# Optimization experiments

Hardware: AMD Instinct MI355X
Metric: run time of the kernel (lower is better)

The kernel has to match this reference:

```python
import jax, jax.numpy as jnp
import numpy as np

# Config constants (match init_kwargs)
D_MODEL = 1024
N_EXPERTS = 8
EXPERT_SCALE = 2          # experts per base group -> n_base_groups = 4
N_FEAT = 16
BANK_DIM = 32
RAW_FEAT = N_FEAT * BANK_DIM   # 512
PROJ_DIM = 256
R_HIDDEN = 256
E_HIDDEN = 256
TOP_K = 2
TEMP = 1.0
LN_EPS = 1e-5


def _layernorm(x, g, b):
    mu = jnp.mean(x, axis=-1, keepdims=True)
    var = jnp.mean((x - mu) ** 2, axis=-1, keepdims=True)
    return (x - mu) * jax.lax.rsqrt(var + LN_EPS) * g + b


def _softmax_top_k(logits, k):
    # keep top-k logits, mask rest to -inf, softmax
    topv = jax.lax.top_k(logits, k)[0]
    thresh = topv[..., -1:]
    masked = jnp.where(logits >= thresh, logits, -jnp.inf)
    return jax.nn.softmax(masked, axis=-1)


def setup_inputs() -> dict:
    key = jax.random.key(0)
    ks = jax.random.split(key, 24)
    B, S = 4, 2048
    s = 0.02
    inp = {
        "hidden": jax.random.normal(ks[0], (B, S, D_MODEL), jnp.float32),
        "feat": jax.random.normal(ks[1], (B, S, N_FEAT), jnp.float32),
        "feat_bank": jax.random.normal(ks[2], (B, S, N_FEAT, BANK_DIM), jnp.float32),
        "item_seq_len": jax.random.randint(ks[3], (B,), 1, S + 1, jnp.int64),
        # pre-LN
        "ln_g": jnp.ones((D_MODEL,), jnp.float32),
        "ln_b": jnp.zeros((D_MODEL,), jnp.float32),
        # router feature projector (2 layers: Linear -> GELU -> Linear)
        "fp_w1": jax.random.normal(ks[4], (RAW_FEAT, PROJ_DIM), jnp.float32) * s,
        "fp_b1": jnp.zeros((PROJ_DIM,), jnp.float32),
        "fp_w2": jax.random.normal(ks[5], (PROJ_DIM, PROJ_DIM), jnp.float32) * s,
        "fp_b2": jnp.zeros((PROJ_DIM,), jnp.float32),
        # learned router MLP: d_in = d_model + proj_dim
        "r_w1": jax.random.normal(ks[6], (D_MODEL + PROJ_DIM, R_HIDDEN), jnp.float32) * s,
        "r_b1": jnp.zeros((R_HIDDEN,), jnp.float32),
        "r_w2": jax.random.normal(ks[7], (R_HIDDEN, N_EXPERTS), jnp.float32) * s,
        "r_b2": jnp.zeros((N_EXPERTS,), jnp.float32),
        # rule router (linear on raw stage features)
        "rr_w": jax.random.normal(ks[8], (N_FEAT, N_EXPERTS), jnp.float32) * s,
        "rr_b": jnp.zeros((N_EXPERTS,), jnp.float32),
        # per-expert FFN
        "e_w1": jax.random.normal(ks[9], (N_EXPERTS, D_MODEL, E_HIDDEN), jnp.float32) * s,
        "e_b1": jnp.zeros((N_EXPERTS, E_HIDDEN), jnp.float32),
        "e_w2": jax.random.normal(ks[10], (N_EXPERTS, E_HIDDEN, D_MODEL), jnp.float32) * s,
        "e_b2": jnp.zeros((N_EXPERTS, D_MODEL), jnp.float32),
        "alpha": jnp.ones((), jnp.float32),
    }
    return inp


def reference(hidden, feat, feat_bank, item_seq_len, ln_g, ln_b,
              fp_w1, fp_b1, fp_w2, fp_b2,
              r_w1, r_b1, r_w2, r_b2,
              rr_w, rr_b,
              e_w1, e_b1, e_w2, e_b2, alpha):
    B, S, D = hidden.shape
    h_norm = _layernorm(hidden, ln_g, ln_b)  # [B,S,D]

    # router feature path: flatten bank, 2-layer GELU projector
    bank_flat = feat_bank.reshape(B, S, RAW_FEAT)
    proj = jnp.dot(jax.nn.gelu(jnp.dot(bank_flat, fp_w1) + fp_b1), fp_w2) + fp_b2  # [B,S,P]

    # token-mode router input: concat hidden + projected features
    router_input = jnp.concatenate([h_norm, proj], axis=-1)
    rule_logits = jnp.dot(feat, rr_w) + rr_b  # rule router on raw stage features

    raw_logits = jnp.dot(jax.nn.gelu(jnp.dot(router_input, r_w1) + r_b1), r_w2) + r_b2
    scaled_logits = raw_logits / max(TEMP, 1e-6)
    gate_weights = _softmax_top_k(scaled_logits, TOP_K)           # [B,S,E]
    rule_target_logits = rule_logits / max(TEMP, 1e-6)

    # expert group: per-expert 2-layer GELU FFN on h_norm
    h1 = jax.nn.gelu(jnp.einsum('bsd,edh->bseh', h_norm, e_w1) + e_b1)
    expert_out = jnp.einsum('bseh,ehd->bsed', h1, e_w2) + e_b2    # [B,S,E,D]

    stage_out = jnp.einsum('bse,bsed->bsd', gate_weights, expert_out)
    next_hidden = hidden + alpha * stage_out

    # _aggregate_group_weights: expert_group_idx = arange(E)//EXPERT_SCALE is
    # contiguous, so gather+sum per group == reshape+sum over the scale axis
    n_groups = N_EXPERTS // EXPERT_SCALE
    group_weights = gate_weights.reshape(B, S, n_groups, EXPERT_SCALE).sum(-1)

    return (next_hidden, stage_out, gate_weights, scaled_logits, group_weights, rule_target_logits)
```

## Files before the change

### kernel.cpp

```cpp
#include <hip/hip_runtime.h>
#include <stdint.h>


typedef unsigned short u16;
using bf16x8 = __attribute__((ext_vector_type(8))) short;
using f32x4  = __attribute__((ext_vector_type(4))) float;

#define WS_HHI 0u
#define WS_HLO 16777216u
#define WS_PB2 33554432u
#define WS_W1T 67108864u
#define WS_IDX 71303168u
#define IX_SELE   0u
#define IX_SELG   65536u
#define IX_ROW    131072u
#define IX_TOKR   196608u
#define IX_GROW   262144u
#define IX_CNT    327680u
#define IX_CBASE  335872u
#define IX_TILEE  344064u
#define IX_TILES  344704u
#define IX_TILEC  345344u
#define IX_META   345984u

__device__ __forceinline__ float gelu_tanh(float x) {
  float x3 = x * x * x;
  float t = tanhf(0.7978845608028654f * (x + 0.044715f * x3));
  return 0.5f * x * (1.0f + t);
}
__device__ __forceinline__ u16 f2bf(float f) {
  uint32_t u = __float_as_uint(f);
  u = u + 0x7fffu + ((u >> 16) & 1u);
  return (u16)(u >> 16);
}
__device__ __forceinline__ float b2f(u16 h) {
  return __uint_as_float(((uint32_t)h) << 16);
}
__device__ __forceinline__ void gll16(const void* g, void* l) {
  __builtin_amdgcn_global_load_lds(
      (const __attribute__((address_space(1))) void*)g,
      (__attribute__((address_space(3))) void*)l, 16, 0, 0);
}

__global__ __launch_bounds__(256) void split_bank_kernel(const float* __restrict__ x,
    u16* __restrict__ hi, u16* __restrict__ lo) {
  int i4 = blockIdx.x * 256 + threadIdx.x;
  float4 v = ((const float4*)x)[i4];
  ushort4 h, l;
  h.x = f2bf(v.x); l.x = f2bf(v.x - b2f(h.x));
  h.y = f2bf(v.y); l.y = f2bf(v.y - b2f(h.y));
  h.z = f2bf(v.z); l.z = f2bf(v.z - b2f(h.z));
  h.w = f2bf(v.w); l.w = f2bf(v.w - b2f(h.w));
  ((ushort4*)hi)[i4] = h;
  ((ushort4*)lo)[i4] = l;
}

__global__ __launch_bounds__(256) void tsplit_kernel(const float* __restrict__ in,
    int inR, int inC, u16* __restrict__ outHi, u16* __restrict__ outLo,
    int outLD, int outColOff) {
  __shared__ u16 hs[64][65];
  __shared__ u16 ls[64][65];
  int tid = threadIdx.x;
  int c0 = blockIdx.x * 64, r0 = blockIdx.y * 64;
  const float* inp = in + (size_t)blockIdx.z * inR * inC;
  int rl = tid >> 6, cl = tid & 63;
#pragma unroll
  for (int p = 0; p < 16; p++) {
    int r = rl + p * 4;
    float v = inp[(size_t)(r0 + r) * inC + c0 + cl];
    u16 h = f2bf(v);
    hs[r][cl] = h;
    ls[r][cl] = f2bf(v - b2f(h));
  }
  __syncthreads();
  size_t obase = (size_t)(blockIdx.z * inC + c0) * outLD + outColOff + r0;
#pragma unroll
  for (int p = 0; p < 16; p++) {
    int c = rl + p * 4;
    outHi[obase + (size_t)c * outLD + cl] = hs[cl][c];
    if (outLo) outLo[obase + (size_t)c * outLD + cl] = ls[cl][c];
  }
}

__global__ __launch_bounds__(256) void wprime_kernel(const float* __restrict__ fp_w2,
    const float* __restrict__ r_w1, const float* __restrict__ fp_b2,
    const float* __restrict__ r_b1, float* __restrict__ wp, float* __restrict__ bp) {
  __shared__ float row[256];
  int i = blockIdx.x, n = threadIdx.x;
  if (i < 256) {
    row[n] = fp_w2[i * 256 + n];
    __syncthreads();
    float acc = 0.0f;
    for (int j = 0; j < 256; j++) acc += row[j] * r_w1[(size_t)(1024 + j) * 256 + n];
    wp[i * 256 + n] = acc;
  } else {
    row[n] = fp_b2[n];
    __syncthreads();
    float acc = r_b1[n];
    for (int j = 0; j < 256; j++) acc += row[j] * r_w1[(size_t)(1024 + j) * 256 + n];
    bp[n] = acc;
  }
}

__global__ __launch_bounds__(256) void ln_kernel(const float* __restrict__ hidden,
    const float* __restrict__ ln_g, const float* __restrict__ ln_b,
    const float* __restrict__ feat, const float* __restrict__ rr_w,
    const float* __restrict__ rr_b,
    u16* __restrict__ h_hi, u16* __restrict__ h_lo, float* __restrict__ rule) {
  int t = blockIdx.x;
  int tid = threadIdx.x;
  float4 v = ((const float4*)(hidden + (size_t)t * 1024))[tid];
  float s = v.x + v.y + v.z + v.w;
#pragma unroll
  for (int o = 32; o > 0; o >>= 1) s += __shfl_down(s, o);
  __shared__ float red[4];
  __shared__ float stats[2];
  int wid = tid >> 6, lane = tid & 63;
  if (lane == 0) red[wid] = s;
  __syncthreads();
  if (tid == 0) stats[0] = (red[0] + red[1] + red[2] + red[3]) * (1.0f / 1024.0f);
  __syncthreads();
  float mu = stats[0];
  float dx = v.x - mu, dy = v.y - mu, dz = v.z - mu, dw = v.w - mu;
  float q = dx * dx + dy * dy + dz * dz + dw * dw;
#pragma unroll
  for (int o = 32; o > 0; o >>= 1) q += __shfl_down(q, o);
  if (lane == 0) red[wid] = q;
  __syncthreads();
  if (tid == 0) {
    float var = (red[0] + red[1] + red[2] + red[3]) * (1.0f / 1024.0f) + 1e-5f;
    float r = rsqrtf(var);
    r = r * (1.5f - 0.5f * var * r * r);
    stats[1] = r;
  }
  __syncthreads();
  float r = stats[1];
  float4 g = ((const float4*)ln_g)[tid];
  float4 b = ((const float4*)ln_b)[tid];
  float4 o;
  o.x = dx * r * g.x + b.x;
  o.y = dy * r * g.y + b.y;
  o.z = dz * r * g.z + b.z;
  o.w = dw * r * g.w + b.w;
  ushort4 hv, lv;
  hv.x = f2bf(o.x); lv.x = f2bf(o.x - b2f(hv.x));
  hv.y = f2bf(o.y); lv.y = f2bf(o.y - b2f(hv.y));
  hv.z = f2bf(o.z); lv.z = f2bf(o.z - b2f(hv.z));
  hv.w = f2bf(o.w); lv.w = f2bf(o.w - b2f(hv.w));
  ((ushort4*)(h_hi + (size_t)t * 1024))[tid] = hv;
  ((ushort4*)(h_lo + (size_t)t * 1024))[tid] = lv;
  if (tid < 8) {
    float acc = rr_b[tid];
#pragma unroll
    for (int f = 0; f < 16; f++) acc += feat[t * 16 + f] * rr_w[f * 8 + tid];
    rule[t * 8 + tid] = acc;
  }
}

__global__ __launch_bounds__(256) void gemm3_kernel(
    const u16* __restrict__ Ah, const u16* __restrict__ Al, int lda,
    int kchunk, int nz1,
    const u16* __restrict__ A2h, const u16* __restrict__ A2l, int lda2,
    int klen2, int bkoff2,
    const u16* __restrict__ Bth, const u16* __restrict__ Btl, int Kb,
    float* __restrict__ parts) {
  __shared__ u16 Ash[128 * 32];
  __shared__ u16 Asl[128 * 32];
  __shared__ u16 Bsh[128 * 32];
  __shared__ u16 Bsl[128 * 32];
  int tid = threadIdx.x;
  int z = blockIdx.z;
  const u16 *pAh, *pAl;
  int lda_, akoff, bkoff, klen;
  if (z < nz1) {
    pAh = Ah; pAl = Al; lda_ = lda; akoff = z * kchunk; bkoff = akoff; klen = kchunk;
  } else {
    pAh = A2h; pAl = A2l; lda_ = lda2; akoff = 0; bkoff = bkoff2; klen = klen2;
  }
  int row0 = blockIdx.y * 128, col0 = blockIdx.x * 128;
  int wave = tid >> 6, lane = tid & 63;
  int wr = (wave >> 1) * 64, wc = (wave & 1) * 64;
  int l16 = lane & 15, qd = lane >> 4;
  f32x4 acc[4][4];
#pragma unroll
  for (int i = 0; i < 4; i++)
#pragma unroll
    for (int j = 0; j < 4; j++) acc[i][j] = 0.0f;

  int r0 = tid >> 2, kc = tid & 3;
  const u16* gAh0 = pAh + (size_t)(row0 + r0) * lda_ + akoff + kc * 8;
  const u16* gAh1 = gAh0 + (size_t)64 * lda_;
  const u16* gAl0 = pAl + (size_t)(row0 + r0) * lda_ + akoff + kc * 8;
  const u16* gAl1 = gAl0 + (size_t)64 * lda_;
  const u16* gBh0 = Bth + (size_t)(col0 + r0) * Kb + bkoff + kc * 8;
  const u16* gBh1 = gBh0 + (size_t)64 * Kb;
  const u16* gBl0 = Btl + (size_t)(col0 + r0) * Kb + bkoff + kc * 8;
  const u16* gBl1 = gBl0 + (size_t)64 * Kb;
  u16* dAh = Ash + tid * 8;
  u16* dAl = Asl + tid * 8;
  u16* dBh = Bsh + tid * 8;
  u16* dBl = Bsl + tid * 8;

  for (int k0 = 0; k0 < klen; k0 += 32) {
    __syncthreads();
    gll16(gAh0 + k0, dAh);
    gll16(gAh1 + k0, dAh + 2048);
    gll16(gAl0 + k0, dAl);
    gll16(gAl1 + k0, dAl + 2048);
    gll16(gBh0 + k0, dBh);
    gll16(gBh1 + k0, dBh + 2048);
    gll16(gBl0 + k0, dBl);
    gll16(gBl1 + k0, dBl + 2048);
    __syncthreads();
    bf16x8 afh[4], afl[4], bfh[4], bfl[4];
#pragma unroll
    for (int i = 0; i < 4; i++) {
      afh[i] = *((const bf16x8*)(Ash + (wr + i * 16 + l16) * 32 + qd * 8));
      afl[i] = *((const bf16x8*)(Asl + (wr + i * 16 + l16) * 32 + qd * 8));
      bfh[i] = *((const bf16x8*)(Bsh + (wc + i * 16 + l16) * 32 + qd * 8));
      bfl[i] = *((const bf16x8*)(Bsl + (wc + i * 16 + l16) * 32 + qd * 8));
    }
#pragma unroll
    for (int i = 0; i < 4; i++)
#pragma unroll
      for (int j = 0; j < 4; j++) {
        acc[i][j] = __builtin_amdgcn_mfma_f32_16x16x32_bf16(afh[i], bfh[j], acc[i][j], 0, 0, 0);
        acc[i][j] = __builtin_amdgcn_mfma_f32_16x16x32_bf16(afl[i], bfh[j], acc[i][j], 0, 0, 0);
        acc[i][j] = __builtin_amdgcn_mfma_f32_16x16x32_bf16(afh[i], bfl[j], acc[i][j], 0, 0, 0);
      }
  }

  float* pz = parts + (size_t)z * 2097152;
#pragma unroll
  for (int i = 0; i < 4; i++)
#pragma unroll
    for (int j = 0; j < 4; j++) {
      int cl = wc + j * 16 + l16;
#pragma unroll
      for (int rr = 0; rr < 4; rr++) {
        int rl = wr + i * 16 + qd * 4 + rr;
        pz[(size_t)(row0 + rl) * 256 + col0 + cl] = acc[i][j][rr];
      }
    }
}

__global__ __launch_bounds__(256) void epi_bf_kernel(const float* __restrict__ parts,
    int nz, const float* __restrict__ bias, int do_gelu,
    u16* __restrict__ hi, u16* __restrict__ lo) {
  int i4 = blockIdx.x * 256 + threadIdx.x;
  float4 s = ((const float4*)parts)[i4];
  for (int zz = 1; zz < nz; zz++) {
    float4 p = ((const float4*)parts)[(size_t)zz * 524288 + i4];
    s.x += p.x; s.y += p.y; s.z += p.z; s.w += p.w;
  }
  float4 bv = ((const float4*)bias)[i4 & 63];
  s.x += bv.x; s.y += bv.y; s.z += bv.z; s.w += bv.w;
  if (do_gelu) {
    s.x = gelu_tanh(s.x); s.y = gelu_tanh(s.y);
    s.z = gelu_tanh(s.z); s.w = gelu_tanh(s.w);
  }
  ushort4 h, l;
  h.x = f2bf(s.x); l.x = f2bf(s.x - b2f(h.x));
  h.y = f2bf(s.y); l.y = f2bf(s.y - b2f(h.y));
  h.z = f2bf(s.z); l.z = f2bf(s.z - b2f(h.z));
  h.w = f2bf(s.w); l.w = f2bf(s.w - b2f(h.w));
  ((ushort4*)hi)[i4] = h;
  ((ushort4*)lo)[i4] = l;
}

__global__ __launch_bounds__(256) void epi_f32_kernel(const float* __restrict__ parts,
    int nz, const float* __restrict__ bias, float* __restrict__ out) {
  int i4 = blockIdx.x * 256 + threadIdx.x;
  float4 s = ((const float4*)parts)[i4];
  for (int zz = 1; zz < nz; zz++) {
    float4 p = ((const float4*)parts)[(size_t)zz * 524288 + i4];
    s.x += p.x; s.y += p.y; s.z += p.z; s.w += p.w;
  }
  float4 bv = ((const float4*)bias)[i4 & 63];
  s.x = gelu_tanh(s.x + bv.x);
  s.y = gelu_tanh(s.y + bv.y);
  s.z = gelu_tanh(s.z + bv.z);
  s.w = gelu_tanh(s.w + bv.w);
  ((float4*)out)[i4] = s;
}

__global__ __launch_bounds__(256) void gate_kernel(const float* __restrict__ r1,
    const float* __restrict__ r_w2, const float* __restrict__ r_b2,
    float* __restrict__ gates, float* __restrict__ slog, float* __restrict__ gw,
    int* __restrict__ selE, float* __restrict__ selG, int* __restrict__ cnt) {
  __shared__ float w2s[2048];
  __shared__ float r1s[32][260];
  __shared__ float lg[32][8];
  __shared__ int se_s[64];
  int tid = threadIdx.x;
  int blk = blockIdx.x;
  int t0 = blk * 32;
  for (int i = tid; i < 2048; i += 256) {
    int e = i >> 8, k = i & 255;
    w2s[i] = r_w2[k * 8 + e];
  }
  for (int i = tid; i < 8192; i += 256) {
    int tt = i >> 8, k = i & 255;
    r1s[tt][k] = r1[(size_t)(t0 + tt) * 256 + k];
  }
  __syncthreads();
  {
    int tl = tid >> 3, e = tid & 7;
    float acc = r_b2[e];
    const float* wrp = &w2s[e * 256];
    const float* rrp = &r1s[tl][0];
    for (int k = 0; k < 256; k += 4) {
      float4 a = *(const float4*)(rrp + k);
      float4 b = *(const float4*)(wrp + k);
      acc += a.x * b.x + a.y * b.y + a.z * b.z + a.w * b.w;
    }
    lg[tl][e] = acc;
  }
  __syncthreads();
  if (tid < 32) {
    int t = t0 + tid;
    float l[8];
#pragma unroll
    for (int i = 0; i < 8; i++) l[i] = lg[tid][i];
    float m1 = -1e30f, m2 = -1e30f;
    int i1 = 0, i2 = 0;
#pragma unroll
    for (int i = 0; i < 8; i++) {
      float v = l[i];
      if (v > m1) { m2 = m1; i2 = i1; m1 = v; i1 = i; }
      else if (v > m2) { m2 = v; i2 = i; }
    }
    float w[8];
    float se = 0.0f;
#pragma unroll
    for (int i = 0; i < 8; i++) {
      float ex = (l[i] >= m2) ? expf(l[i] - m1) : 0.0f;
      w[i] = ex;
      se += ex;
    }
    float inv = 1.0f / se;
#pragma unroll
    for (int i = 0; i < 8; i++) {
      gates[(size_t)t * 8 + i] = w[i] * inv;
      slog[(size_t)t * 8 + i] = l[i];
    }
#pragma unroll
    for (int gi = 0; gi < 4; gi++)
      gw[(size_t)t * 4 + gi] = (w[2 * gi] + w[2 * gi + 1]) * inv;
    se_s[tid * 2] = i1;
    se_s[tid * 2 + 1] = i2;
    selE[t * 2] = i1;      selG[t * 2] = w[i1] * inv;
    selE[t * 2 + 1] = i2;  selG[t * 2 + 1] = w[i2] * inv;
  }
  __syncthreads();
  if (tid < 8) {
    int c = 0;
#pragma unroll
    for (int s = 0; s < 64; s++) c += (se_s[s] == tid) ? 1 : 0;
    cnt[blk * 8 + tid] = c;
  }
}

__global__ __launch_bounds__(256) void stageb_kernel(const int* __restrict__ cnt,
    int* __restrict__ cbase, int* __restrict__ tileE, int* __restrict__ tileS,
    int* __restrict__ tileC, int* __restrict__ meta) {
  __shared__ int cs[2048];
  __shared__ int tot[8];
  __shared__ int ebase[8];
  int tid = threadIdx.x;
  for (int i = tid; i < 2048; i += 256) cs[i] = cnt[i];
  __syncthreads();
  if (tid < 8) {
    int s = 0;
    for (int c = 0; c < 256; c++) s += cs[c * 8 + tid];
    tot[tid] = s;
  }
  __syncthreads();
  if (tid == 0) {
    int b = 0, nt = 0;
    for (int e = 0; e < 8; e++) {
      ebase[e] = b;
      int c = tot[e];
      for (int off = 0; off < c; off += 128) {
        tileE[nt] = e; tileS[nt] = b + off;
        tileC[nt] = (c - off < 128) ? (c - off) : 128;
        nt++;
      }
      b += c;
    }
    meta[16] = nt;
  }
  __syncthreads();
  if (tid < 8) {
    int run = ebase[tid];
    for (int c = 0; c < 256; c++) {
      cbase[c * 8 + tid] = run;
      run += cs[c * 8 + tid];
    }
  }
}

__global__ __launch_bounds__(256) void scatter_kernel(const int* __restrict__ selE,
    const float* __restrict__ selG, const int* __restrict__ cbase,
    int* __restrict__ rowsel, int* __restrict__ tokrow, float* __restrict__ grow) {
  int chunk = blockIdx.x;
  int wave = threadIdx.x >> 6, lane = threadIdx.x & 63;
  int slot = chunk * 64 + lane;
  int sel = selE[slot];
  float g = selG[slot];
  int tokn = chunk * 32 + (lane >> 1);
  unsigned long long lt = (1ULL << lane) - 1ULL;
#pragma unroll
  for (int ei = 0; ei < 2; ei++) {
    int e = wave + ei * 4;
    unsigned long long m = __ballot(sel == e);
    if (sel == e) {
      int row = cbase[chunk * 8 + e] + __popcll(m & lt);
      rowsel[slot] = row;
      tokrow[row] = tokn;
      grow[row] = g;
    }
  }
}

__global__ __launch_bounds__(256) void gexp1_kernel(const u16* __restrict__ A,
    const u16* __restrict__ w1t, const float* __restrict__ e_b1,
    const int* __restrict__ tokrow, const float* __restrict__ grow,
    const int* __restrict__ tileE, const int* __restrict__ tileS,
    const int* __restrict__ tileC, const int* __restrict__ meta,
    u16* __restrict__ pb1) {
  int ty = blockIdx.y;
  if (ty >= meta[16]) return;
  int e = tileE[ty], pstart = tileS[ty], pcnt = tileC[ty];
  if (pcnt <= 0) return;
  __shared__ u16 As[128 * 32];
  __shared__ u16 Bs[128 * 32];
  __shared__ float gsl[128];
  int tid = threadIdx.x;
  int col0 = blockIdx.x * 128;
  if (tid < 128) {
    int rr = (tid < pcnt) ? tid : (pcnt - 1);
    gsl[tid] = grow[pstart + rr];
  }
  int wave = tid >> 6, lane = tid & 63;
  int wr = (wave >> 1) * 64, wc = (wave & 1) * 64;
  int l16 = lane & 15, qd = lane >> 4;
  f32x4 acc[4][4];
#pragma unroll
  for (int i = 0; i < 4; i++)
#pragma unroll
    for (int j = 0; j < 4; j++) acc[i][j] = 0.0f;

  int r0 = tid >> 2, kc = tid & 3;
  int ra = (r0 < pcnt) ? r0 : (pcnt - 1);
  int rb = (r0 + 64 < pcnt) ? (r0 + 64) : (pcnt - 1);
  int ta = tokrow[pstart + ra];
  int tb = tokrow[pstart + rb];
  const u16* Ap0 = A + (size_t)ta * 1024 + kc * 8;
  const u16* Ap1 = A + (size_t)tb * 1024 + kc * 8;
  const u16* Bp0 = w1t + (size_t)(e * 256 + col0 + r0) * 1024 + kc * 8;
  const u16* Bp1 = Bp0 + (size_t)64 * 1024;
  u16* dA = As + tid * 8;
  u16* dB = Bs + tid * 8;

  for (int k0 = 0; k0 < 1024; k0 += 32) {
    __syncthreads();
    gll16(Ap0 + k0, dA);
    gll16(Ap1 + k0, dA + 2048);
    gll16(Bp0 + k0, dB);
    gll16(Bp1 + k0, dB + 2048);
    __syncthreads();
    bf16x8 af[4], bfr[4];
#pragma unroll
    for (int i = 0; i < 4; i++) {
      af[i]  = *((const bf16x8*)(As + (wr + i * 16 + l16) * 32 + qd * 8));
      bfr[i] = *((const bf16x8*)(Bs + (wc + i * 16 + l16) * 32 + qd * 8));
    }
#pragma unroll
    for (int i = 0; i < 4; i++)
#pragma unroll
      for (int j = 0; j < 4; j++)
        acc[i][j] = __builtin_amdgcn_mfma_f32_16x16x32_bf16(af[i], bfr[j], acc[i][j], 0, 0, 0);
  }

#pragma unroll
  for (int i = 0; i < 4; i++)
#pragma unroll
    for (int j = 0; j < 4; j++) {
      int cl = wc + j * 16 + l16;
      int col = col0 + cl;
      float bcol = e_b1[e * 256 + col];
#pragma unroll
      for (int rr = 0; rr < 4; rr++) {
        int rl = wr + i * 16 + qd * 4 + rr;
        if (rl < pcnt) {
          float v = gelu_tanh(acc[i][j][rr] + bcol) * gsl[rl];
          pb1[(size_t)(pstart + rl) * 256 + col] = f2bf(v);
        }
      }
    }
}

__global__ __launch_bounds__(256) void gexp2_kernel(const u16* __restrict__ pb1,
    const u16* __restrict__ w2te,
    const int* __restrict__ tileE, const int* __restrict__ tileS,
    const int* __restrict__ tileC, const int* __restrict__ meta,
    u16* __restrict__ pb2) {
  int ty = blockIdx.y;
  if (ty >= meta[16]) return;
  int e = tileE[ty], pstart = tileS[ty], pcnt = tileC[ty];
  if (pcnt <= 0) return;
  __shared__ u16 As[128 * 32];
  __shared__ u16 Bs[128 * 32];
  int tid = threadIdx.x;
  int col0 = blockIdx.x * 128;
  int wave = tid >> 6, lane = tid & 63;
  int wr = (wave >> 1) * 64, wc = (wave & 1) * 64;
  int l16 = lane & 15, qd = lane >> 4;
  f32x4 acc[4][4];
#pragma unroll
  for (int i = 0; i < 4; i++)
#pragma unroll
    for (int j = 0; j < 4; j++) acc[i][j] = 0.0f;

  int r0 = tid >> 2, kc = tid & 3;
  int ra = (r0 < pcnt) ? r0 : (pcnt - 1);
  int rb = (r0 + 64 < pcnt) ? (r0 + 64) : (pcnt - 1);
  const u16* Ap0 = pb1 + (size_t)(pstart + ra) * 256 + kc * 8;
  const u16* Ap1 = pb1 + (size_t)(pstart + rb) * 256 + kc * 8;
  const u16* Bp0 = w2te + (size_t)(e * 1024 + col0 + r0) * 256 + kc * 8;
  const u16* Bp1 = Bp0 + (size_t)64 * 256;
  u16* dA = As + tid * 8;
  u16* dB = Bs + tid * 8;

  for (int k0 = 0; k0 < 256; k0 += 32) {
    __syncthreads();
    gll16(Ap0 + k0, dA);
    gll16(Ap1 + k0, dA + 2048);
    gll16(Bp0 + k0, dB);
    gll16(Bp1 + k0, dB + 2048);
    __syncthreads();
    bf16x8 af[4], bfr[4];
#pragma unroll
    for (int i = 0; i < 4; i++) {
      af[i]  = *((const bf16x8*)(As + (wr + i * 16 + l16) * 32 + qd * 8));
      bfr[i] = *((const bf16x8*)(Bs + (wc + i * 16 + l16) * 32 + qd * 8));
    }
#pragma unroll
    for (int i = 0; i < 4; i++)
#pragma unroll
      for (int j = 0; j < 4; j++)
        acc[i][j] = __builtin_amdgcn_mfma_f32_16x16x32_bf16(af[i], bfr[j], acc[i][j], 0, 0, 0);
  }

#pragma unroll
  for (int i = 0; i < 4; i++)
#pragma unroll
    for (int j = 0; j < 4; j++) {
      int cl = wc + j * 16 + l16;
#pragma unroll
      for (int rr = 0; rr < 4; rr++) {
        int rl = wr + i * 16 + qd * 4 + rr;
        if (rl < pcnt)
          pb2[(size_t)(pstart + rl) * 1024 + col0 + cl] = f2bf(acc[i][j][rr]);
      }
    }
}

__global__ __launch_bounds__(256) void combine_kernel(const u16* __restrict__ pb2,
    const int* __restrict__ rowsel, const int* __restrict__ selE,
    const float* __restrict__ selG, const float* __restrict__ e_b2,
    const float* __restrict__ hidden, const float* __restrict__ alpha_p,
    float* __restrict__ stage, float* __restrict__ next) {
  int t = blockIdx.x;
  int c = threadIdx.x * 4;
  int rA = rowsel[t * 2], rB = rowsel[t * 2 + 1];
  int eA = selE[t * 2], eB = selE[t * 2 + 1];
  float gA = selG[t * 2], gB = selG[t * 2 + 1];
  float al = alpha_p[0];
  ushort4 pa = *((const ushort4*)(pb2 + (size_t)rA * 1024 + c));
  ushort4 pb = *((const ushort4*)(pb2 + (size_t)rB * 1024 + c));
  float4 ba = *((const float4*)(e_b2 + (size_t)eA * 1024 + c));
  float4 bb = *((const float4*)(e_b2 + (size_t)eB * 1024 + c));
  float4 h = *((const float4*)(hidden + (size_t)t * 1024 + c));
  float4 v;
  v.x = b2f(pa.x) + b2f(pb.x) + gA * ba.x + gB * bb.x;
  v.y = b2f(pa.y) + b2f(pb.y) + gA * ba.y + gB * bb.y;
  v.z = b2f(pa.z) + b2f(pb.z) + gA * ba.z + gB * bb.z;
  v.w = b2f(pa.w) + b2f(pb.w) + gA * ba.w + gB * bb.w;
  *((float4*)(stage + (size_t)t * 1024 + c)) = v;
  float4 n;
  n.x = h.x + al * v.x; n.y = h.y + al * v.y;
  n.z = h.z + al * v.z; n.w = h.w + al * v.w;
  *((float4*)(next + (size_t)t * 1024 + c)) = n;
}

extern "C" void kernel_launch(void* const* d_in, const int* in_sizes, int n_in,
                              void* d_out, int out_size, void* d_ws, size_t ws_size,
                              hipStream_t stream) {
  const float* hidden    = (const float*)d_in[0];
  const float* feat      = (const float*)d_in[1];
  const float* feat_bank = (const float*)d_in[2];
  const float* ln_g  = (const float*)d_in[4];
  const float* ln_b  = (const float*)d_in[5];
  const float* fp_w1 = (const float*)d_in[6];
  const float* fp_b1 = (const float*)d_in[7];
  const float* fp_w2 = (const float*)d_in[8];
  const float* fp_b2 = (const float*)d_in[9];
  const float* r_w1  = (const float*)d_in[10];
  const float* r_b1  = (const float*)d_in[11];
  const float* r_w2  = (const float*)d_in[12];
  const float* r_b2  = (const float*)d_in[13];
  const float* rr_w  = (const float*)d_in[14];
  const float* rr_b  = (const float*)d_in[15];
  const float* e_w1  = (const float*)d_in[16];
  const float* e_b1  = (const float*)d_in[17];
  const float* e_w2  = (const float*)d_in[18];
  const float* e_b2  = (const float*)d_in[19];
  const float* alpha = (const float*)d_in[20];

  char* ob = (char*)d_out;
  float* next  = (float*)ob;
  float* stage = (float*)(ob + 33554432);
  float* gates = (float*)(ob + 67108864);
  float* slog  = gates + 65536;
  float* gw    = slog + 65536;
  float* rule  = gw + 32768;

  u16* bank_hi  = (u16*)ob;
  u16* bank_lo  = (u16*)(ob + 8388608);
  float* r1     = (float*)ob;
  u16* fpw1t_hi = (u16*)(ob + 16777216);
  u16* fpw1t_lo = (u16*)(ob + 17039360);
  float* wp     = (float*)(ob + 17301504);
  float* bp     = (float*)(ob + 17563648);
  u16* rw1t_hi  = (u16*)(ob + 17825792);
  u16* rw1t_lo  = (u16*)(ob + 18481152);
  u16* mid_hi   = (u16*)(ob + 19136512);
  u16* mid_lo   = (u16*)(ob + 23330816);
  u16* w2te     = (u16*)(ob + 19136512);

  char* sb = ob + 33554432;
  float* parts = (float*)sb;
  u16* pb1     = (u16*)sb;

  char* ws = (char*)d_ws;
  u16* h_hi = (u16*)(ws + WS_HHI);
  u16* h_lo = (u16*)(ws + WS_HLO);
  u16* pb2  = (u16*)(ws + WS_PB2);
  u16* w1t  = (u16*)(ws + WS_W1T);
  char* ix  = ws + WS_IDX;
  int*   selE   = (int*)(ix + IX_SELE);
  float* selG   = (float*)(ix + IX_SELG);
  int*   rowsel = (int*)(ix + IX_ROW);
  int*   tokrow = (int*)(ix + IX_TOKR);
  float* grow   = (float*)(ix + IX_GROW);
  int*   cnt    = (int*)(ix + IX_CNT);
  int*   cbase  = (int*)(ix + IX_CBASE);
  int*   tileE  = (int*)(ix + IX_TILEE);
  int*   tileS  = (int*)(ix + IX_TILES);
  int*   tileC  = (int*)(ix + IX_TILEC);
  int*   meta   = (int*)(ix + IX_META);

  split_bank_kernel<<<4096, 256, 0, stream>>>(feat_bank, bank_hi, bank_lo);
  wprime_kernel<<<257, 256, 0, stream>>>(fp_w2, r_w1, fp_b2, r_b1, wp, bp);
  tsplit_kernel<<<dim3(4, 8, 1), 256, 0, stream>>>(fp_w1, 512, 256,
      fpw1t_hi, fpw1t_lo, 512, 0);
  tsplit_kernel<<<dim3(4, 16, 1), 256, 0, stream>>>(r_w1, 1024, 256,
      rw1t_hi, rw1t_lo, 1280, 0);
  tsplit_kernel<<<dim3(4, 4, 1), 256, 0, stream>>>(wp, 256, 256,
      rw1t_hi, rw1t_lo, 1280, 1024);
  tsplit_kernel<<<dim3(4, 16, 8), 256, 0, stream>>>(e_w1, 1024, 256,
      w1t, nullptr, 1024, 0);
  ln_kernel<<<8192, 256, 0, stream>>>(hidden, ln_g, ln_b, feat, rr_w, rr_b,
                                      h_hi, h_lo, rule);
  gemm3_kernel<<<dim3(2, 64, 4), 256, 0, stream>>>(
      bank_hi, bank_lo, 512, 128, 4,
      bank_hi, bank_lo, 512, 0, 0,
      fpw1t_hi, fpw1t_lo, 512, parts);
  epi_bf_kernel<<<2048, 256, 0, stream>>>(parts, 4, fp_b1, 1, mid_hi, mid_lo);
  gemm3_kernel<<<dim3(2, 64, 3), 256, 0, stream>>>(
      h_hi, h_lo, 1024, 512, 2,
      mid_hi, mid_lo, 256, 256, 1024,
      rw1t_hi, rw1t_lo, 1280, parts);
  tsplit_kernel<<<dim3(16, 4, 8), 256, 0, stream>>>(e_w2, 256, 1024,
      w2te, nullptr, 256, 0);
  epi_f32_kernel<<<2048, 256, 0, stream>>>(parts, 3, bp, r1);
  gate_kernel<<<256, 256, 0, stream>>>(r1, r_w2, r_b2, gates, slog, gw,
      selE, selG, cnt);
  stageb_kernel<<<1, 256, 0, stream>>>(cnt, cbase, tileE, tileS, tileC, meta);
  scatter_kernel<<<256, 256, 0, stream>>>(selE, selG, cbase, rowsel, tokrow, grow);
  gexp1_kernel<<<dim3(2, 136), 256, 0, stream>>>(h_hi, w1t, e_b1, tokrow, grow,
      tileE, tileS, tileC, meta, pb1);
  gexp2_kernel<<<dim3(8, 136), 256, 0, stream>>>(pb1, w2te, tileE, tileS, tileC,
      meta, pb2);
  combine_kernel<<<8192, 256, 0, stream>>>(pb2, rowsel, selE, selG, e_b2,
      hidden, alpha, stage, next);
}
```

Measured before the change: 361.3 us.

## Retile first expert GEMM into 64x64 double-buffered swizzled tiles

The first grouped expert GEMM moves from 128x128 tiles over a 2D grid to 64x64 tiles over a 1D grid of 1152 blocks. A second tile list with 64-row granularity is built in the scheduling kernel to drive it. The K loop is now double-buffered so global-to-LDS loads overlap the MFMAs, and an XOR swizzle is applied to the LDS layout to reduce bank conflicts. The intent is more parallelism and less padding waste for this small-M grouped GEMM, at the cost of more B-matrix reloads per output and extra launch overhead for blocks that exit early.

```diff
diff --git a/kernel.cpp b/kernel.cpp
--- a/kernel.cpp
+++ b/kernel.cpp
@@ -22,6 +22,9 @@
 #define IX_TILES  344704u
 #define IX_TILEC  345344u
 #define IX_META   345984u
+#define IX_TILEE2 346112u
+#define IX_TILES2 347264u
+#define IX_TILEC2 348416u
 
 __device__ __forceinline__ float gelu_tanh(float x) {
   float x3 = x * x * x;
@@ -363,7 +366,8 @@
 
 __global__ __launch_bounds__(256) void stageb_kernel(const int* __restrict__ cnt,
     int* __restrict__ cbase, int* __restrict__ tileE, int* __restrict__ tileS,
-    int* __restrict__ tileC, int* __restrict__ meta) {
+    int* __restrict__ tileC, int* __restrict__ tileE2, int* __restrict__ tileS2,
+    int* __restrict__ tileC2, int* __restrict__ meta) {
   __shared__ int cs[2048];
   __shared__ int tot[8];
   __shared__ int ebase[8];
@@ -389,6 +393,17 @@
       b += c;
     }
     meta[16] = nt;
+    int b2 = 0, nt2 = 0;
+    for (int e = 0; e < 8; e++) {
+      int c = tot[e];
+      for (int off = 0; off < c; off += 64) {
+        tileE2[nt2] = e; tileS2[nt2] = b2 + off;
+        tileC2[nt2] = (c - off < 64) ? (c - off) : 64;
+        nt2++;
+      }
+      b2 += c;
+    }
+    meta[17] = nt2;
   }
   __syncthreads();
   if (tid < 8) {
@@ -426,75 +441,95 @@
 __global__ __launch_bounds__(256) void gexp1_kernel(const u16* __restrict__ A,
     const u16* __restrict__ w1t, const float* __restrict__ e_b1,
     const int* __restrict__ tokrow, const float* __restrict__ grow,
-    const int* __restrict__ tileE, const int* __restrict__ tileS,
-    const int* __restrict__ tileC, const int* __restrict__ meta,
+    const int* __restrict__ tileE2, const int* __restrict__ tileS2,
+    const int* __restrict__ tileC2, const int* __restrict__ meta,
     u16* __restrict__ pb1) {
-  int ty = blockIdx.y;
-  if (ty >= meta[16]) return;
-  int e = tileE[ty], pstart = tileS[ty], pcnt = tileC[ty];
-  if (pcnt <= 0) return;
-  __shared__ u16 As[128 * 32];
-  __shared__ u16 Bs[128 * 32];
-  __shared__ float gsl[128];
+  __shared__ u16 As0[64 * 32];
+  __shared__ u16 As1[64 * 32];
+  __shared__ u16 Bs0[64 * 32];
+  __shared__ u16 Bs1[64 * 32];
+  __shared__ float gsl[64];
+  int n = blockIdx.x;
+  int ty = ((n >> 5) << 3) + (n & 7);
+  int cblk = (n >> 3) & 3;
+  if (ty >= meta[17]) return;
+  int e = tileE2[ty], pstart = tileS2[ty], pcnt = tileC2[ty];
   int tid = threadIdx.x;
-  int col0 = blockIdx.x * 128;
-  if (tid < 128) {
+  int col0 = cblk * 64;
+  if (tid < 64) {
     int rr = (tid < pcnt) ? tid : (pcnt - 1);
     gsl[tid] = grow[pstart + rr];
   }
   int wave = tid >> 6, lane = tid & 63;
-  int wr = (wave >> 1) * 64, wc = (wave & 1) * 64;
+  int wr = (wave >> 1) * 32, wc = (wave & 1) * 32;
   int l16 = lane & 15, qd = lane >> 4;
-  f32x4 acc[4][4];
-#pragma unroll
-  for (int i = 0; i < 4; i++)
-#pragma unroll
-    for (int j = 0; j < 4; j++) acc[i][j] = 0.0f;
+  int xq = qd ^ ((l16 >> 1) & 3);
+  f32x4 acc[2][2];
+  acc[0][0] = 0.0f; acc[0][1] = 0.0f; acc[1][0] = 0.0f; acc[1][1] = 0.0f;
 
   int r0 = tid >> 2, kc = tid & 3;
+  int kcs = kc ^ ((r0 >> 1) & 3);
   int ra = (r0 < pcnt) ? r0 : (pcnt - 1);
-  int rb = (r0 + 64 < pcnt) ? (r0 + 64) : (pcnt - 1);
   int ta = tokrow[pstart + ra];
-  int tb = tokrow[pstart + rb];
-  const u16* Ap0 = A + (size_t)ta * 1024 + kc * 8;
-  const u16* Ap1 = A + (size_t)tb * 1024 + kc * 8;
-  const u16* Bp0 = w1t + (size_t)(e * 256 + col0 + r0) * 1024 + kc * 8;
-  const u16* Bp1 = Bp0 + (size_t)64 * 1024;
-  u16* dA = As + tid * 8;
-  u16* dB = Bs + tid * 8;
-
-  for (int k0 = 0; k0 < 1024; k0 += 32) {
-    __syncthreads();
-    gll16(Ap0 + k0, dA);
-    gll16(Ap1 + k0, dA + 2048);
-    gll16(Bp0 + k0, dB);
-    gll16(Bp1 + k0, dB + 2048);
-    __syncthreads();
-    bf16x8 af[4], bfr[4];
-#pragma unroll
-    for (int i = 0; i < 4; i++) {
-      af[i]  = *((const bf16x8*)(As + (wr + i * 16 + l16) * 32 + qd * 8));
-      bfr[i] = *((const bf16x8*)(Bs + (wc + i * 16 + l16) * 32 + qd * 8));
-    }
-#pragma unroll
-    for (int i = 0; i < 4; i++)
-#pragma unroll
-      for (int j = 0; j < 4; j++)
-        acc[i][j] = __builtin_amdgcn_mfma_f32_16x16x32_bf16(af[i], bfr[j], acc[i][j], 0, 0, 0);
-  }
-
-#pragma unroll
-  for (int i = 0; i < 4; i++)
-#pragma unroll
-    for (int j = 0; j < 4; j++) {
+  const u16* Ap = A + (size_t)ta * 1024 + kcs * 8;
+  const u16* Bp = w1t + (size_t)(e * 256 + col0 + r0) * 1024 + kcs * 8;
+  u16* dA0 = As0 + tid * 8;
+  u16* dA1 = As1 + tid * 8;
+  u16* dB0 = Bs0 + tid * 8;
+  u16* dB1 = Bs1 + tid * 8;
+
+  int aoff0 = (wr + l16) * 32 + xq * 8;
+  int aoff1 = aoff0 + 16 * 32;
+  int boff0 = (wc + l16) * 32 + xq * 8;
+  int boff1 = boff0 + 16 * 32;
+
+  gll16(Ap, dA0);
+  gll16(Bp, dB0);
+  __syncthreads();
+
+  for (int k0 = 0; k0 < 1024; k0 += 64) {
+    {
+      gll16(Ap + k0 + 32, dA1);
+      gll16(Bp + k0 + 32, dB1);
+      bf16x8 a0 = *((const bf16x8*)(As0 + aoff0));
+      bf16x8 a1 = *((const bf16x8*)(As0 + aoff1));
+      bf16x8 b0 = *((const bf16x8*)(Bs0 + boff0));
+      bf16x8 b1 = *((const bf16x8*)(Bs0 + boff1));
+      acc[0][0] = __builtin_amdgcn_mfma_f32_16x16x32_bf16(a0, b0, acc[0][0], 0, 0, 0);
+      acc[0][1] = __builtin_amdgcn_mfma_f32_16x16x32_bf16(a0, b1, acc[0][1], 0, 0, 0);
+      acc[1][0] = __builtin_amdgcn_mfma_f32_16x16x32_bf16(a1, b0, acc[1][0], 0, 0, 0);
+      acc[1][1] = __builtin_amdgcn_mfma_f32_16x16x32_bf16(a1, b1, acc[1][1], 0, 0, 0);
+      __syncthreads();
+    }
+    {
+      if (k0 + 64 < 1024) {
+        gll16(Ap + k0 + 64, dA0);
+        gll16(Bp + k0 + 64, dB0);
+      }
+      bf16x8 a0 = *((const bf16x8*)(As1 + aoff0));
+      bf16x8 a1 = *((const bf16x8*)(As1 + aoff1));
+      bf16x8 b0 = *((const bf16x8*)(Bs1 + boff0));
+      bf16x8 b1 = *((const bf16x8*)(Bs1 + boff1));
+      acc[0][0] = __builtin_amdgcn_mfma_f32_16x16x32_bf16(a0, b0, acc[0][0], 0, 0, 0);
+      acc[0][1] = __builtin_amdgcn_mfma_f32_16x16x32_bf16(a0, b1, acc[0][1], 0, 0, 0);
+      acc[1][0] = __builtin_amdgcn_mfma_f32_16x16x32_bf16(a1, b0, acc[1][0], 0, 0, 0);
+      acc[1][1] = __builtin_amdgcn_mfma_f32_16x16x32_bf16(a1, b1, acc[1][1], 0, 0, 0);
+      __syncthreads();
+    }
+  }
+
+#pragma unroll
+  for (int i = 0; i < 2; i++)
+#pragma unroll
+    for (int j = 0; j < 2; j++) {
       int cl = wc + j * 16 + l16;
       int col = col0 + cl;
-      float bcol = e_b1[e * 256 + col];
+      float bc = e_b1[e * 256 + col];
 #pragma unroll
       for (int rr = 0; rr < 4; rr++) {
         int rl = wr + i * 16 + qd * 4 + rr;
         if (rl < pcnt) {
-          float v = gelu_tanh(acc[i][j][rr] + bcol) * gsl[rl];
+          float v = gelu_tanh(acc[i][j][rr] + bc) * gsl[rl];
           pb1[(size_t)(pstart + rl) * 256 + col] = f2bf(v);
         }
       }
@@ -660,6 +695,9 @@
   int*   tileE  = (int*)(ix + IX_TILEE);
   int*   tileS  = (int*)(ix + IX_TILES);
   int*   tileC  = (int*)(ix + IX_TILEC);
+  int*   tileE2 = (int*)(ix + IX_TILEE2);
+  int*   tileS2 = (int*)(ix + IX_TILES2);
+  int*   tileC2 = (int*)(ix + IX_TILEC2);
   int*   meta   = (int*)(ix + IX_META);
 
   split_bank_kernel<<<4096, 256, 0, stream>>>(feat_bank, bank_hi, bank_lo);
@@ -688,10 +726,11 @@
   epi_f32_kernel<<<2048, 256, 0, stream>>>(parts, 3, bp, r1);
   gate_kernel<<<256, 256, 0, stream>>>(r1, r_w2, r_b2, gates, slog, gw,
       selE, selG, cnt);
-  stageb_kernel<<<1, 256, 0, stream>>>(cnt, cbase, tileE, tileS, tileC, meta);
+  stageb_kernel<<<1, 256, 0, stream>>>(cnt, cbase, tileE, tileS, tileC,
+      tileE2, tileS2, tileC2, meta);
   scatter_kernel<<<256, 256, 0, stream>>>(selE, selG, cbase, rowsel, tokrow, grow);
-  gexp1_kernel<<<dim3(2, 136), 256, 0, stream>>>(h_hi, w1t, e_b1, tokrow, grow,
-      tileE, tileS, tileC, meta, pb1);
+  gexp1_kernel<<<1152, 256, 0, stream>>>(h_hi, w1t, e_b1, tokrow, grow,
+      tileE2, tileS2, tileC2, meta, pb1);
   gexp2_kernel<<<dim3(8, 136), 256, 0, stream>>>(pb1, w2te, tileE, tileS, tileC,
       meta, pb2);
   combine_kernel<<<8192, 256, 0, stream>>>(pb2, rowsel, selE, selG, e_b2,
```

New measurement: 356.0 us. No clear change (-1.5%).
